# Kernel tuning notes

Measured on AMD Instinct MI355X. Metric: run time of the kernel, lower is better.

The kernel has to match this reference:

```python
import jax, jax.numpy as jnp
import numpy as np

N, E, G = 50000, 640000, 256
NODE_IN, EDGE_IN, H, L, T = 64, 16, 128, 4, 5
BN_EPS = 1e-5

def setup_inputs() -> dict:
    key = jax.random.key(0)
    ks = jax.random.split(key, 24)
    s = lambda k, shape, fan: jax.random.normal(k, shape, jnp.float32) * (1.0 / np.sqrt(fan))
    return {
        "x": jax.random.normal(ks[0], (N, NODE_IN), jnp.float32),
        "edge_attr": jax.random.normal(ks[1], (E, EDGE_IN), jnp.float32),
        "node_w": s(ks[2], (NODE_IN, H), NODE_IN), "node_b": jnp.zeros((H,), jnp.float32),
        "edge_w1": s(ks[3], (EDGE_IN, H), EDGE_IN), "edge_b1": jnp.zeros((H,), jnp.float32),
        "edge_w2": s(ks[4], (H, H), H), "edge_b2": jnp.zeros((H,), jnp.float32),
        "conv_w1": s(ks[5], (L, H, H), H), "conv_b1": jnp.zeros((L, H), jnp.float32),
        "conv_w2": s(ks[6], (L, H, H), H), "conv_b2": jnp.zeros((L, H), jnp.float32),
        "bn_gamma": jnp.ones((L, H), jnp.float32), "bn_beta": jnp.zeros((L, H), jnp.float32),
        "gate_w1": s(ks[7], (H, H // 2), H), "gate_b1": jnp.zeros((H // 2,), jnp.float32),
        "gate_w2": s(ks[8], (H // 2, 1), H // 2), "gate_b2": jnp.zeros((1,), jnp.float32),
        "head_w1": s(ks[9], (H, H), H), "head_b1": jnp.zeros((H,), jnp.float32),
        "head_w2": s(ks[10], (H, T), H), "head_b2": jnp.zeros((T,), jnp.float32),
        "edge_index": jax.random.randint(ks[11], (2, E), 0, N, jnp.int32),
        "batch": jnp.sort(jax.random.randint(ks[12], (N,), 0, G, jnp.int32)),
    }

def reference(x, edge_attr, node_w, node_b, edge_w1, edge_b1, edge_w2, edge_b2,
              conv_w1, conv_b1, conv_w2, conv_b2, bn_gamma, bn_beta,
              gate_w1, gate_b1, gate_w2, gate_b2, head_w1, head_b1, head_w2, head_b2,
              edge_index, batch):
    relu = jax.nn.relu
    h = x @ node_w + node_b                                   # [N,H]
    e = relu(edge_attr @ edge_w1 + edge_b1) @ edge_w2 + edge_b2  # [E,H]
    src, dst = edge_index[0], edge_index[1]
    bn_scale = 1.0 / jnp.sqrt(jnp.float32(1.0) + BN_EPS)      # eval BN: mean=0, var=1
    for l in range(L):
        m = relu(h[src] + e)                                  # GINEConv message [E,H]
        aggr = jax.ops.segment_sum(m, dst, num_segments=N)    # scatter-add
        z = h + aggr                                          # eps=0: (1+eps)*x + aggr
        z = relu(z @ conv_w1[l] + conv_b1[l]) @ conv_w2[l] + conv_b2[l]
        z = z * bn_scale * bn_gamma[l] + bn_beta[l]
        h = relu(z)                                           # dropout off (eval)
    gate = relu(h @ gate_w1 + gate_b1) @ gate_w2 + gate_b2    # [N,1]
    gmax = jax.ops.segment_max(gate, batch, num_segments=G)   # segment softmax
    wexp = jnp.exp(gate - gmax[batch])
    denom = jax.ops.segment_sum(wexp, batch, num_segments=G)
    alpha = wexp / denom[batch]
    g = jax.ops.segment_sum(alpha * h, batch, num_segments=G) # [G,H]
    return relu(g @ head_w1 + head_b1) @ head_w2 + head_b2    # [G,T]
```

## Files before the change

kernel.cpp:

```cpp
#include <hip/hip_runtime.h>

typedef unsigned short u16;
typedef __bf16 bf16x8 __attribute__((ext_vector_type(8)));
typedef float f32x4 __attribute__((ext_vector_type(4)));
typedef unsigned short u16x8 __attribute__((ext_vector_type(8)));

#define NNODES 50000
#define NEDGES 640000
#define NGRAPH 256

__device__ __forceinline__ float bf2f(u16 u) {
  unsigned int v = ((unsigned int)u) << 16; float f; __builtin_memcpy(&f, &v, 4); return f;
}
__device__ __forceinline__ u16 f2bf(float f) {
  unsigned int x; __builtin_memcpy(&x, &f, 4);
  unsigned int lsb = (x >> 16) & 1u;
  x += 0x7fffu + lsb;
  return (u16)(x >> 16);
}

__global__ void write_zero_f32(float* __restrict__ out, int n) {
  int i = blockIdx.x * 256 + threadIdx.x;
  if (i < n) out[i] = 0.f;
}

__global__ void prep_weights(const float* __restrict__ node_w, const float* __restrict__ edge_w1,
                             const float* __restrict__ edge_w2, const float* __restrict__ conv_w1,
                             const float* __restrict__ conv_w2, const float* __restrict__ gate_w1,
                             u16* __restrict__ node_wt, u16* __restrict__ edge_w1t,
                             u16* __restrict__ edge_w2t, u16* __restrict__ conv_w1t,
                             u16* __restrict__ conv_w2t, u16* __restrict__ gate_w1t,
                             int* __restrict__ counts, int* __restrict__ gcounts) {
  int o = blockIdx.x * 256 + threadIdx.x;
  if (o < NNODES) counts[o] = 0;
  if (o < NGRAPH) gcounts[o] = 0;
  if (o < 8192) { int n = o >> 6, k = o & 63; node_wt[o] = f2bf(node_w[k * 128 + n]); return; }
  o -= 8192;
  if (o < 4096) { int n = o >> 5, k = o & 31;
                  edge_w1t[o] = (k < 16) ? f2bf(edge_w1[k * 128 + n]) : (u16)0; return; }
  o -= 4096;
  if (o < 16384) { int n = o >> 7, k = o & 127; edge_w2t[o] = f2bf(edge_w2[k * 128 + n]); return; }
  o -= 16384;
  if (o < 65536) { int l = o >> 14, r = o & 16383, n = r >> 7, k = r & 127;
                   conv_w1t[o] = f2bf(conv_w1[l * 16384 + k * 128 + n]); return; }
  o -= 65536;
  if (o < 65536) { int l = o >> 14, r = o & 16383, n = r >> 7, k = r & 127;
                   conv_w2t[o] = f2bf(conv_w2[l * 16384 + k * 128 + n]); return; }
  o -= 65536;
  if (o < 8192) { int n = o >> 7, k = o & 127; gate_w1t[o] = f2bf(gate_w1[k * 64 + n]); }
}

__global__ void hist_all(const int* __restrict__ dst, const int* __restrict__ b,
                         int* __restrict__ counts, int* __restrict__ gc, int n) {
  int i = blockIdx.x * 256 + threadIdx.x;
  atomicAdd(&counts[dst[i]], 1);
  if (i < n) atomicAdd(&gc[b[i]], 1);
}
__global__ void scan_a(const int* __restrict__ counts, int* __restrict__ bsums,
                       const int* __restrict__ gcounts, int* __restrict__ goffs, int n) {
  __shared__ int sh4[4];
  int b = blockIdx.x, t = threadIdx.x;
  int lane = t & 63, w = t >> 6;
  if (b == 49) {
    int v = gcounts[t];
    int x = v;
    for (int d = 1; d < 64; d <<= 1) { int y = __shfl_up(x, (unsigned)d, 64); if (lane >= d) x += y; }
    if (lane == 63) sh4[w] = x;
    __syncthreads();
    int add = 0;
    for (int i = 0; i < w; i++) add += sh4[i];
    int incl = add + x;
    goffs[t] = incl - v;
    if (t == 255) goffs[256] = incl;
    return;
  }
  int i0 = b * 1024 + t * 4;
  int s = 0;
#pragma unroll
  for (int j = 0; j < 4; j++) { int i = i0 + j; if (i < n) s += counts[i]; }
  for (int m = 32; m; m >>= 1) s += __shfl_xor(s, m, 64);
  if (lane == 0) sh4[w] = s;
  __syncthreads();
  if (t == 0) bsums[b] = sh4[0] + sh4[1] + sh4[2] + sh4[3];
}
__global__ void scan_c(const int* __restrict__ counts, const int* __restrict__ bsums,
                       int* __restrict__ offs, int* __restrict__ cursor, int n) {
  int b = blockIdx.x, t = threadIdx.x;
  int i0 = b * 1024 + t * 4;
  int v[4]; int s = 0;
#pragma unroll
  for (int j = 0; j < 4; j++) { v[j] = (i0 + j < n) ? counts[i0 + j] : 0; s += v[j]; }
  int lane = t & 63, w = t >> 6;
  int x = s;
  for (int d = 1; d < 64; d <<= 1) { int y = __shfl_up(x, (unsigned)d, 64); if (lane >= d) x += y; }
  __shared__ int wt_[4];
  if (lane == 63) wt_[w] = x;
  __syncthreads();
  int add = 0;
  for (int i = 0; i < b; i++) add += bsums[i];
  for (int i = 0; i < w; i++) add += wt_[i];
  int excl = add + x - s;
#pragma unroll
  for (int j = 0; j < 4; j++) {
    int i = i0 + j;
    if (i < n) { offs[i] = excl; cursor[i] = excl; }
    excl += v[j];
  }
  if (b == 0 && t == 0) offs[n] = NEDGES;
}
__global__ void scatter_csr(const int* __restrict__ src, const int* __restrict__ dst,
                            int* __restrict__ cursor, int* __restrict__ csr_src,
                            int* __restrict__ csr_eid) {
  int i = blockIdx.x * 256 + threadIdx.x;
  int d = dst[i];
  int p = atomicAdd(&cursor[d], 1);
  csr_src[p] = src[i];
  csr_eid[p] = i;
}

template <int KB, int SA, int SB>
__device__ __forceinline__ void mfma_block(const u16* aL, const u16* bL, int m, int quad,
                                           int rbase, f32x4* acc) {
#pragma unroll
  for (int kb = 0; kb < KB; ++kb) {
    bf16x8 a = *(const bf16x8*)(aL + (rbase + m) * SA + kb * 32 + quad * 8);
#pragma unroll
    for (int nt = 0; nt < 8; ++nt) {
      bf16x8 b = *(const bf16x8*)(bL + (nt * 16 + m) * SB + kb * 32 + quad * 8);
      acc[nt] = __builtin_amdgcn_mfma_f32_16x16x32_bf16(a, b, acc[nt], 0, 0, 0);
    }
  }
}

__global__ __launch_bounds__(256) void node_encode(const float* __restrict__ x,
                                                   const u16* __restrict__ wt,
                                                   const float* __restrict__ nb,
                                                   u16* __restrict__ hb, int n) {
  __shared__ alignas(16) u16 sA[64 * 72];
  __shared__ alignas(16) u16 sW[128 * 72];
  int t = threadIdx.x;
  int row0 = blockIdx.x * 64;
#pragma unroll
  for (int i = 0; i < 4; i++) {
    int idx = t + 256 * i; int r = idx >> 4, c = idx & 15;
    int grow = row0 + r; if (grow > n - 1) grow = n - 1;
    float4 v = *(const float4*)(x + (size_t)grow * 64 + c * 4);
    ushort4 o; o.x = f2bf(v.x); o.y = f2bf(v.y); o.z = f2bf(v.z); o.w = f2bf(v.w);
    *(ushort4*)&sA[r * 72 + c * 4] = o;
  }
#pragma unroll
  for (int i = 0; i < 4; i++) {
    int idx = t + 256 * i; int nr = idx >> 3, c = idx & 7;
    *(uint4*)&sW[nr * 72 + c * 8] = *(const uint4*)(wt + nr * 64 + c * 8);
  }
  __syncthreads();
  int lane = t & 63, w = t >> 6, m = lane & 15, quad = lane >> 4, rbase = w * 16;
  f32x4 acc[8];
  f32x4 z4 = {0.f, 0.f, 0.f, 0.f};
#pragma unroll
  for (int i = 0; i < 8; i++) acc[i] = z4;
  mfma_block<2, 72, 72>(sA, sW, m, quad, rbase, acc);
#pragma unroll
  for (int nt = 0; nt < 8; nt++) {
    int col = nt * 16 + m;
    float bb = nb[col];
    f32x4 a4 = acc[nt];
#pragma unroll
    for (int r = 0; r < 4; r++) {
      int grow = row0 + rbase + quad * 4 + r;
      if (grow < n) hb[(size_t)grow * 128 + col] = f2bf(a4[r] + bb);
    }
  }
}

__global__ __launch_bounds__(256) void edge_encode(const float* __restrict__ ea,
                                                   const u16* __restrict__ w1t,
                                                   const u16* __restrict__ w2t,
                                                   const float* __restrict__ b1,
                                                   const float* __restrict__ b2,
                                                   const int* __restrict__ csr_eid,
                                                   u16* __restrict__ e_perm) {
  __shared__ alignas(16) u16 sA[128 * 48];
  __shared__ alignas(16) u16 sMid[128 * 136];
  int t = threadIdx.x;
  int lane = t & 63, w = t >> 6, m = lane & 15, quad = lane >> 4;
  int s0 = blockIdx.x * 128;
  int ebase = w * 32;

  {
    int r = lane >> 1, c = lane & 1;
    uint4 z = {0, 0, 0, 0};
    *(uint4*)&sA[(ebase + r) * 48 + 16 + c * 8] = z;
    int eidv = 0;
    if (lane < 32) eidv = csr_eid[s0 + ebase + lane];
    int eid = __shfl(eidv, r, 64);
    float4 v0 = *(const float4*)(ea + (size_t)eid * 16 + c * 8);
    float4 v1 = *(const float4*)(ea + (size_t)eid * 16 + c * 8 + 4);
    ushort4 o0; o0.x = f2bf(v0.x); o0.y = f2bf(v0.y); o0.z = f2bf(v0.z); o0.w = f2bf(v0.w);
    ushort4 o1; o1.x = f2bf(v1.x); o1.y = f2bf(v1.y); o1.z = f2bf(v1.z); o1.w = f2bf(v1.w);
    *(ushort4*)&sA[(ebase + r) * 48 + c * 8] = o0;
    *(ushort4*)&sA[(ebase + r) * 48 + c * 8 + 4] = o1;
  }
  bf16x8 w1f[8];
#pragma unroll
  for (int nt = 0; nt < 8; nt++)
    w1f[nt] = *(const bf16x8*)(w1t + (nt * 16 + m) * 32 + quad * 8);

  f32x4 z4 = {0.f, 0.f, 0.f, 0.f};
  f32x4 acc1[16];
#pragma unroll
  for (int i = 0; i < 16; i++) acc1[i] = z4;
#pragma unroll
  for (int rt2 = 0; rt2 < 2; rt2++) {
    bf16x8 a = *(const bf16x8*)(&sA[(ebase + rt2 * 16 + m) * 48 + quad * 8]);
#pragma unroll
    for (int nt = 0; nt < 8; nt++)
      acc1[rt2 * 8 + nt] = __builtin_amdgcn_mfma_f32_16x16x32_bf16(w1f[nt], a, acc1[rt2 * 8 + nt], 0, 0, 0);
  }
#pragma unroll
  for (int rt2 = 0; rt2 < 2; rt2++) {
#pragma unroll
    for (int nt = 0; nt < 8; nt++) {
      float4 bb = *(const float4*)&b1[nt * 16 + quad * 4];
      f32x4 a4 = acc1[rt2 * 8 + nt];
      u16 q0 = f2bf(fmaxf(a4[0] + bb.x, 0.f));
      u16 q1 = f2bf(fmaxf(a4[1] + bb.y, 0.f));
      u16 q2 = f2bf(fmaxf(a4[2] + bb.z, 0.f));
      u16 q3 = f2bf(fmaxf(a4[3] + bb.w, 0.f));
      uint2 pk;
      pk.x = (unsigned int)q0 | ((unsigned int)q1 << 16);
      pk.y = (unsigned int)q2 | ((unsigned int)q3 << 16);
      *(uint2*)&sMid[(ebase + rt2 * 16 + m) * 136 + nt * 16 + quad * 4] = pk;
    }
  }
  bf16x8 w2f[8];
  float4 b2v[2];
#pragma unroll
  for (int ct = 0; ct < 2; ct++) {
    b2v[ct] = *(const float4*)&b2[w * 32 + ct * 16 + quad * 4];
#pragma unroll
    for (int kb = 0; kb < 4; kb++)
      w2f[ct * 4 + kb] = *(const bf16x8*)(w2t + (size_t)(w * 32 + ct * 16 + m) * 128 + kb * 32 + quad * 8);
  }
  __syncthreads();

  f32x4 acc2[16];
#pragma unroll
  for (int i = 0; i < 16; i++) acc2[i] = z4;
#pragma unroll
  for (int rt = 0; rt < 8; rt++) {
#pragma unroll
    for (int kb = 0; kb < 4; kb++) {
      bf16x8 a = *(const bf16x8*)(&sMid[(rt * 16 + m) * 136 + kb * 32 + quad * 8]);
      acc2[rt * 2 + 0] = __builtin_amdgcn_mfma_f32_16x16x32_bf16(w2f[kb], a, acc2[rt * 2 + 0], 0, 0, 0);
      acc2[rt * 2 + 1] = __builtin_amdgcn_mfma_f32_16x16x32_bf16(w2f[4 + kb], a, acc2[rt * 2 + 1], 0, 0, 0);
    }
  }
  __syncthreads();
#pragma unroll
  for (int rt = 0; rt < 8; rt++) {
#pragma unroll
    for (int ct = 0; ct < 2; ct++) {
      f32x4 a4 = acc2[rt * 2 + ct];
      u16 q0 = f2bf(a4[0] + b2v[ct].x);
      u16 q1 = f2bf(a4[1] + b2v[ct].y);
      u16 q2 = f2bf(a4[2] + b2v[ct].z);
      u16 q3 = f2bf(a4[3] + b2v[ct].w);
      uint2 pk;
      pk.x = (unsigned int)q0 | ((unsigned int)q1 << 16);
      pk.y = (unsigned int)q2 | ((unsigned int)q3 << 16);
      *(uint2*)&sMid[(rt * 16 + m) * 136 + w * 32 + ct * 16 + quad * 4] = pk;
    }
  }
  __syncthreads();
#pragma unroll
  for (int i = 0; i < 8; i++) {
    int idx = t + 256 * i; int r = idx >> 4, c = idx & 15;
    *(uint4*)(e_perm + (size_t)(s0 + r) * 128 + c * 8) = *(const uint4*)&sMid[r * 136 + c * 8];
  }
}

__global__ __launch_bounds__(256) void layer_k(const u16* __restrict__ hin,
                                               u16* __restrict__ hout,
                                               const u16* __restrict__ e_perm,
                                               const int* __restrict__ offs,
                                               const int* __restrict__ csr_src,
                                               const u16* __restrict__ w1t, const u16* __restrict__ w2t,
                                               const float* __restrict__ b1, const float* __restrict__ b2,
                                               const float* __restrict__ gam, const float* __restrict__ bet,
                                               int n) {
  __shared__ alignas(16) u16 sZ[64 * 136];
  __shared__ alignas(16) u16 sMid[64 * 136];
  int t = threadIdx.x;
  int lane = t & 63, w = t >> 6, m = lane & 15, quad = lane >> 4;
  int row0 = blockIdx.x * 64;
  int li = m, q = quad;

  for (int k = 0; k < 16; k++) {
    int lr = w * 16 + k;
    int nd = row0 + lr; if (nd > n - 1) nd = n - 1;
    int e0 = offs[nd], e1 = offs[nd + 1];
    u16x8 hv = {};
    if (q == 0) hv = *(const u16x8*)(hin + (size_t)nd * 128 + li * 8);
    float a[8];
#pragma unroll
    for (int j = 0; j < 8; j++) a[j] = 0.f;
    int s = e0 + q;
    for (; s + 8 <= e1; s += 8) {
      int v0 = csr_src[s], v1 = csr_src[s + 4];
      u16x8 h0 = *(const u16x8*)(hin + (size_t)v0 * 128 + li * 8);
      u16x8 ee0 = *(const u16x8*)(e_perm + (size_t)s * 128 + li * 8);
      u16x8 h1 = *(const u16x8*)(hin + (size_t)v1 * 128 + li * 8);
      u16x8 ee1 = *(const u16x8*)(e_perm + (size_t)(s + 4) * 128 + li * 8);
#pragma unroll
      for (int j = 0; j < 8; j++) {
        a[j] += fmaxf(bf2f(h0[j]) + bf2f(ee0[j]), 0.f);
        a[j] += fmaxf(bf2f(h1[j]) + bf2f(ee1[j]), 0.f);
      }
    }
    for (; s < e1; s += 4) {
      int v = csr_src[s];
      u16x8 hgv = *(const u16x8*)(hin + (size_t)v * 128 + li * 8);
      u16x8 ev = *(const u16x8*)(e_perm + (size_t)s * 128 + li * 8);
#pragma unroll
      for (int j = 0; j < 8; j++) a[j] += fmaxf(bf2f(hgv[j]) + bf2f(ev[j]), 0.f);
    }
#pragma unroll
    for (int j = 0; j < 8; j++) {
      a[j] += __shfl_xor(a[j], 16, 64);
      a[j] += __shfl_xor(a[j], 32, 64);
    }
    if (q == 0) {
      u16x8 o;
#pragma unroll
      for (int j = 0; j < 8; j++) o[j] = f2bf(bf2f(hv[j]) + a[j]);
      *(u16x8*)&sZ[lr * 136 + li * 8] = o;
    }
  }
  bf16x8 w1f[8];
  float4 b1v[2];
#pragma unroll
  for (int ct = 0; ct < 2; ct++) {
    b1v[ct] = *(const float4*)&b1[w * 32 + ct * 16 + quad * 4];
#pragma unroll
    for (int kb = 0; kb < 4; kb++)
      w1f[ct * 4 + kb] = *(const bf16x8*)(w1t + (size_t)(w * 32 + ct * 16 + m) * 128 + kb * 32 + quad * 8);
  }
  __syncthreads();

  f32x4 z4 = {0.f, 0.f, 0.f, 0.f};
  f32x4 acc[8];
#pragma unroll
  for (int i = 0; i < 8; i++) acc[i] = z4;
#pragma unroll
  for (int rt = 0; rt < 4; rt++) {
#pragma unroll
    for (int kb = 0; kb < 4; kb++) {
      bf16x8 a = *(const bf16x8*)(&sZ[(rt * 16 + m) * 136 + kb * 32 + quad * 8]);
      acc[rt * 2 + 0] = __builtin_amdgcn_mfma_f32_16x16x32_bf16(w1f[kb], a, acc[rt * 2 + 0], 0, 0, 0);
      acc[rt * 2 + 1] = __builtin_amdgcn_mfma_f32_16x16x32_bf16(w1f[4 + kb], a, acc[rt * 2 + 1], 0, 0, 0);
    }
  }
#pragma unroll
  for (int rt = 0; rt < 4; rt++) {
#pragma unroll
    for (int ct = 0; ct < 2; ct++) {
      f32x4 a4 = acc[rt * 2 + ct];
      u16 q0 = f2bf(fmaxf(a4[0] + b1v[ct].x, 0.f));
      u16 q1 = f2bf(fmaxf(a4[1] + b1v[ct].y, 0.f));
      u16 q2 = f2bf(fmaxf(a4[2] + b1v[ct].z, 0.f));
      u16 q3 = f2bf(fmaxf(a4[3] + b1v[ct].w, 0.f));
      uint2 pk;
      pk.x = (unsigned int)q0 | ((unsigned int)q1 << 16);
      pk.y = (unsigned int)q2 | ((unsigned int)q3 << 16);
      *(uint2*)&sMid[(rt * 16 + m) * 136 + w * 32 + ct * 16 + quad * 4] = pk;
    }
  }
  bf16x8 w2f[8];
  float4 b2v[2], gamv[2], betv[2];
#pragma unroll
  for (int ct = 0; ct < 2; ct++) {
    int c0 = w * 32 + ct * 16 + quad * 4;
    b2v[ct] = *(const float4*)&b2[c0];
    gamv[ct] = *(const float4*)&gam[c0];
    betv[ct] = *(const float4*)&bet[c0];
#pragma unroll
    for (int kb = 0; kb < 4; kb++)
      w2f[ct * 4 + kb] = *(const bf16x8*)(w2t + (size_t)c0 / 4 * 0 + (size_t)(w * 32 + ct * 16 + m) * 128 + kb * 32 + quad * 8);
  }
  __syncthreads();

  f32x4 acc2[8];
#pragma unroll
  for (int i = 0; i < 8; i++) acc2[i] = z4;
#pragma unroll
  for (int rt = 0; rt < 4; rt++) {
#pragma unroll
    for (int kb = 0; kb < 4; kb++) {
      bf16x8 a = *(const bf16x8*)(&sMid[(rt * 16 + m) * 136 + kb * 32 + quad * 8]);
      acc2[rt * 2 + 0] = __builtin_amdgcn_mfma_f32_16x16x32_bf16(w2f[kb], a, acc2[rt * 2 + 0], 0, 0, 0);
      acc2[rt * 2 + 1] = __builtin_amdgcn_mfma_f32_16x16x32_bf16(w2f[4 + kb], a, acc2[rt * 2 + 1], 0, 0, 0);
    }
  }
  const float bns = 0.99999500003749983f;
#pragma unroll
  for (int rt = 0; rt < 4; rt++) {
#pragma unroll
    for (int ct = 0; ct < 2; ct++) {
      f32x4 a4 = acc2[rt * 2 + ct];
      u16 q0 = f2bf(fmaxf((a4[0] + b2v[ct].x) * bns * gamv[ct].x + betv[ct].x, 0.f));
      u16 q1 = f2bf(fmaxf((a4[1] + b2v[ct].y) * bns * gamv[ct].y + betv[ct].y, 0.f));
      u16 q2 = f2bf(fmaxf((a4[2] + b2v[ct].z) * bns * gamv[ct].z + betv[ct].z, 0.f));
      u16 q3 = f2bf(fmaxf((a4[3] + b2v[ct].w) * bns * gamv[ct].w + betv[ct].w, 0.f));
      uint2 pk;
      pk.x = (unsigned int)q0 | ((unsigned int)q1 << 16);
      pk.y = (unsigned int)q2 | ((unsigned int)q3 << 16);
      *(uint2*)&sZ[(rt * 16 + m) * 136 + w * 32 + ct * 16 + quad * 4] = pk;
    }
  }
  __syncthreads();
#pragma unroll
  for (int i = 0; i < 4; i++) {
    int idx = t + 256 * i; int r = idx >> 4, c = idx & 15;
    int grow = row0 + r;
    if (grow < n)
      *(uint4*)(hout + (size_t)grow * 128 + c * 8) = *(const uint4*)&sZ[r * 136 + c * 8];
  }
}

__global__ __launch_bounds__(256) void gate_k(const u16* __restrict__ hb,
                                              const u16* __restrict__ w1t,
                                              const float* __restrict__ b1,
                                              const float* __restrict__ w2,
                                              const float* __restrict__ b2,
                                              float* __restrict__ gate, int n) {
  __shared__ alignas(16) u16 sA[64 * 136];
  __shared__ alignas(16) u16 sW[64 * 136];
  int t = threadIdx.x;
  int row0 = blockIdx.x * 64;
#pragma unroll
  for (int i = 0; i < 4; i++) {
    int idx = t + 256 * i; int r = idx >> 4, c = idx & 15;
    int grow = row0 + r; if (grow > n - 1) grow = n - 1;
    *(uint4*)&sA[r * 136 + c * 8] = *(const uint4*)(hb + (size_t)grow * 128 + c * 8);
  }
#pragma unroll
  for (int i = 0; i < 4; i++) {
    int idx = t + 256 * i; int r = idx >> 4, c = idx & 15;
    *(uint4*)&sW[r * 136 + c * 8] = *(const uint4*)(w1t + r * 128 + c * 8);
  }
  __syncthreads();
  int lane = t & 63, w = t >> 6, m = lane & 15, quad = lane >> 4, rbase = w * 16;
  f32x4 z4 = {0.f, 0.f, 0.f, 0.f};
  f32x4 acc[4];
#pragma unroll
  for (int i = 0; i < 4; i++) acc[i] = z4;
#pragma unroll
  for (int kb = 0; kb < 4; kb++) {
    bf16x8 a = *(const bf16x8*)(&sA[(rbase + m) * 136 + kb * 32 + quad * 8]);
#pragma unroll
    for (int nt = 0; nt < 4; nt++) {
      bf16x8 b = *(const bf16x8*)(&sW[(nt * 16 + m) * 136 + kb * 32 + quad * 8]);
      acc[nt] = __builtin_amdgcn_mfma_f32_16x16x32_bf16(a, b, acc[nt], 0, 0, 0);
    }
  }
  float b1v[4], w2v[4];
#pragma unroll
  for (int nt = 0; nt < 4; nt++) { b1v[nt] = b1[nt * 16 + m]; w2v[nt] = w2[nt * 16 + m]; }
  float b2v = b2[0];
#pragma unroll
  for (int r = 0; r < 4; r++) {
    float p = 0.f;
#pragma unroll
    for (int nt = 0; nt < 4; nt++) p += fmaxf(acc[nt][r] + b1v[nt], 0.f) * w2v[nt];
    p += __shfl_xor(p, 1, 64);
    p += __shfl_xor(p, 2, 64);
    p += __shfl_xor(p, 4, 64);
    p += __shfl_xor(p, 8, 64);
    if (m == 0) {
      int grow = row0 + rbase + quad * 4 + r;
      if (grow < n) gate[grow] = p + b2v;
    }
  }
}

__global__ __launch_bounds__(256) void pool_k(const float* __restrict__ gate,
                                              const u16* __restrict__ hb,
                                              const int* __restrict__ goffs,
                                              float* __restrict__ gpool) {
  int g = blockIdx.x, t = threadIdx.x;
  int s0 = goffs[g], s1 = goffs[g + 1];
  int lane = t & 63, w = t >> 6;
  __shared__ float red[4];
  __shared__ float fin[2][128];
  float mx = -3.4e38f;
  for (int i = s0 + t; i < s1; i += 256) mx = fmaxf(mx, gate[i]);
  for (int d = 32; d; d >>= 1) mx = fmaxf(mx, __shfl_xor(mx, d, 64));
  if (lane == 0) red[w] = mx;
  __syncthreads();
  mx = fmaxf(fmaxf(red[0], red[1]), fmaxf(red[2], red[3]));
  __syncthreads();
  float sm = 0.f;
  for (int i = s0 + t; i < s1; i += 256) sm += __expf(gate[i] - mx);
  for (int d = 32; d; d >>= 1) sm += __shfl_xor(sm, d, 64);
  if (lane == 0) red[w] = sm;
  __syncthreads();
  sm = red[0] + red[1] + red[2] + red[3];
  int g2 = t >> 7, tc = t & 127;
  float acc = 0.f;
  for (int i = s0 + g2; i < s1; i += 2)
    acc += __expf(gate[i] - mx) * bf2f(hb[(size_t)i * 128 + tc]);
  fin[g2][tc] = acc;
  __syncthreads();
  if (t < 128) gpool[g * 128 + t] = (s1 > s0) ? (fin[0][t] + fin[1][t]) / sm : 0.f;
}

__global__ __launch_bounds__(128) void head_k(const float* __restrict__ gpool,
                                              const float* __restrict__ w1, const float* __restrict__ b1,
                                              const float* __restrict__ w2, const float* __restrict__ b2,
                                              float* __restrict__ out) {
  int g = blockIdx.x, t = threadIdx.x;
  __shared__ float sg[128];
  __shared__ float shid[128];
  sg[t] = gpool[g * 128 + t];
  __syncthreads();
  float s = 0.f;
  for (int k = 0; k < 128; k++) s += sg[k] * w1[k * 128 + t];
  shid[t] = fmaxf(s + b1[t], 0.f);
  __syncthreads();
  if (t < 5) {
    float o = b2[t];
    for (int k = 0; k < 128; k++) o += shid[k] * w2[k * 5 + t];
    out[g * 5 + t] = o;
  }
}

extern "C" void kernel_launch(void* const* d_in, const int* in_sizes, int n_in,
                              void* d_out, int out_size, void* d_ws, size_t ws_size,
                              hipStream_t stream) {
  const int N = NNODES, E = NEDGES, G = NGRAPH;
  const float* x = (const float*)d_in[0];
  const float* edge_attr = (const float*)d_in[1];
  const float* node_w = (const float*)d_in[2];
  const float* node_b = (const float*)d_in[3];
  const float* edge_w1 = (const float*)d_in[4];
  const float* edge_b1 = (const float*)d_in[5];
  const float* edge_w2 = (const float*)d_in[6];
  const float* edge_b2 = (const float*)d_in[7];
  const float* conv_w1 = (const float*)d_in[8];
  const float* conv_b1 = (const float*)d_in[9];
  const float* conv_w2 = (const float*)d_in[10];
  const float* conv_b2 = (const float*)d_in[11];
  const float* bn_gamma = (const float*)d_in[12];
  const float* bn_beta = (const float*)d_in[13];
  const float* gate_w1 = (const float*)d_in[14];
  const float* gate_b1 = (const float*)d_in[15];
  const float* gate_w2 = (const float*)d_in[16];
  const float* gate_b2 = (const float*)d_in[17];
  const float* head_w1 = (const float*)d_in[18];
  const float* head_b1 = (const float*)d_in[19];
  const float* head_w2 = (const float*)d_in[20];
  const float* head_b2 = (const float*)d_in[21];
  const int* eidx = (const int*)d_in[22];
  const int* batch = (const int*)d_in[23];
  const int* esrc = eidx;
  const int* edst = eidx + E;

  char* wp = (char*)d_ws;
  auto alloc = [&](size_t bytes) { char* p = wp; wp += (bytes + 255) & ~(size_t)255; return p; };
  u16* e_perm = (u16*)alloc((size_t)E * 128 * 2);
  u16* hb = (u16*)alloc((size_t)(N + 16) * 128 * 2);
  u16* hb2 = (u16*)alloc((size_t)(N + 16) * 128 * 2);
  float* gate = (float*)alloc((size_t)N * 4);
  float* gpool = (float*)alloc((size_t)G * 128 * 4);
  int* counts = (int*)alloc((size_t)N * 4);
  int* offs = (int*)alloc((size_t)(N + 1) * 4);
  int* cursor = (int*)alloc((size_t)N * 4);
  int* csr_src = (int*)alloc((size_t)E * 4);
  int* csr_eid = (int*)alloc((size_t)E * 4);
  int* bsums = (int*)alloc(64 * 4);
  int* gcounts = (int*)alloc(G * 4);
  int* goffs = (int*)alloc((G + 1) * 4);
  u16* node_wt = (u16*)alloc(8192 * 2);
  u16* edge_w1t = (u16*)alloc(4096 * 2);
  u16* edge_w2t = (u16*)alloc(16384 * 2);
  u16* conv_w1t = (u16*)alloc(65536 * 2);
  u16* conv_w2t = (u16*)alloc(65536 * 2);
  u16* gate_w1t = (u16*)alloc(8192 * 2);

  size_t need = (size_t)(wp - (char*)d_ws);
  if (need > ws_size) {
    write_zero_f32<<<(out_size + 255) / 256, 256, 0, stream>>>((float*)d_out, out_size);
    return;
  }

  prep_weights<<<656, 256, 0, stream>>>(node_w, edge_w1, edge_w2, conv_w1, conv_w2, gate_w1,
                                        node_wt, edge_w1t, edge_w2t, conv_w1t, conv_w2t, gate_w1t,
                                        counts, gcounts);
  hist_all<<<E / 256, 256, 0, stream>>>(edst, batch, counts, gcounts, N);
  scan_a<<<50, 256, 0, stream>>>(counts, bsums, gcounts, goffs, N);
  scan_c<<<49, 256, 0, stream>>>(counts, bsums, offs, cursor, N);
  scatter_csr<<<E / 256, 256, 0, stream>>>(esrc, edst, cursor, csr_src, csr_eid);
  node_encode<<<(N + 63) / 64, 256, 0, stream>>>(x, node_wt, node_b, hb, N);
  edge_encode<<<E / 128, 256, 0, stream>>>(edge_attr, edge_w1t, edge_w2t, edge_b1, edge_b2,
                                           csr_eid, e_perm);
  u16* hcur = hb;
  u16* hnext = hb2;
  for (int l = 0; l < 4; l++) {
    layer_k<<<(N + 63) / 64, 256, 0, stream>>>(hcur, hnext, e_perm, offs, csr_src,
                                               conv_w1t + l * 16384, conv_w2t + l * 16384,
                                               conv_b1 + l * 128, conv_b2 + l * 128,
                                               bn_gamma + l * 128, bn_beta + l * 128, N);
    u16* tmp = hcur; hcur = hnext; hnext = tmp;
  }
  gate_k<<<(N + 63) / 64, 256, 0, stream>>>(hcur, gate_w1t, gate_b1, gate_w2, gate_b2, gate, N);
  pool_k<<<G, 256, 0, stream>>>(gate, hcur, goffs, gpool);
  head_k<<<G, 128, 0, stream>>>(gpool, head_w1, head_b1, head_w2, head_b2, (float*)d_out);
}
```

Baseline: 646.2 us.

## Build CSR with chunked shared-memory histograms instead of global atomics

Replaces the global-atomic histogram and cursor-based scatter with a two-level scheme. Blocks own a 4096-node chunk and one of 16 edge slices, count destinations in LDS, and write per-slice partial counts that scan_a turns into per-slice offsets. The scatter then places edges using LDS atomics, which also makes the CSR order deterministic. Graph offsets now come from a binary search on the sorted batch array, and layer_k loads its row offsets once per wave and broadcasts them with shuffles. In exchange, each of the 13 chunks rescans the whole dst array in both hist and scatter, and the partial array adds 16×N ints of traffic.

```diff
diff --git a/kernel.cpp b/kernel.cpp
--- a/kernel.cpp
+++ b/kernel.cpp
@@ -8,6 +8,9 @@
 #define NNODES 50000
 #define NEDGES 640000
 #define NGRAPH 256
+#define HCHUNK 4096
+#define HSPLIT 16
+#define NCHUNK 13
 
 __device__ __forceinline__ float bf2f(u16 u) {
   unsigned int v = ((unsigned int)u) << 16; float f; __builtin_memcpy(&f, &v, 4); return f;
@@ -29,11 +32,8 @@
                              const float* __restrict__ conv_w2, const float* __restrict__ gate_w1,
                              u16* __restrict__ node_wt, u16* __restrict__ edge_w1t,
                              u16* __restrict__ edge_w2t, u16* __restrict__ conv_w1t,
-                             u16* __restrict__ conv_w2t, u16* __restrict__ gate_w1t,
-                             int* __restrict__ counts, int* __restrict__ gcounts) {
+                             u16* __restrict__ conv_w2t, u16* __restrict__ gate_w1t) {
   int o = blockIdx.x * 256 + threadIdx.x;
-  if (o < NNODES) counts[o] = 0;
-  if (o < NGRAPH) gcounts[o] = 0;
   if (o < 8192) { int n = o >> 6, k = o & 63; node_wt[o] = f2bf(node_w[k * 128 + n]); return; }
   o -= 8192;
   if (o < 4096) { int n = o >> 5, k = o & 31;
@@ -50,41 +50,65 @@
   if (o < 8192) { int n = o >> 7, k = o & 127; gate_w1t[o] = f2bf(gate_w1[k * 64 + n]); }
 }
 
-__global__ void hist_all(const int* __restrict__ dst, const int* __restrict__ b,
-                         int* __restrict__ counts, int* __restrict__ gc, int n) {
-  int i = blockIdx.x * 256 + threadIdx.x;
-  atomicAdd(&counts[dst[i]], 1);
-  if (i < n) atomicAdd(&gc[b[i]], 1);
-}
-__global__ void scan_a(const int* __restrict__ counts, int* __restrict__ bsums,
-                       const int* __restrict__ gcounts, int* __restrict__ goffs, int n) {
+__global__ __launch_bounds__(256) void hist_k(const int* __restrict__ dst,
+                                              int* __restrict__ partial) {
+  __shared__ int hloc[HCHUNK];
+  int b = blockIdx.x, t = threadIdx.x;
+  int c = b >> 4, sp = b & 15;
+  for (int j = t; j < HCHUNK; j += 256) hloc[j] = 0;
+  __syncthreads();
+  int base = c * HCHUNK;
+  int e0 = sp * (NEDGES / HSPLIT), e1 = e0 + NEDGES / HSPLIT;
+  for (int i = e0 + t; i < e1; i += 256) {
+    int d = dst[i] - base;
+    if ((unsigned)d < HCHUNK) atomicAdd(&hloc[d], 1);
+  }
+  __syncthreads();
+  for (int j = t; j < HCHUNK; j += 256) {
+    int g = base + j;
+    if (g < NNODES) partial[sp * NNODES + g] = hloc[j];
+  }
+}
+__global__ __launch_bounds__(256) void scan_a(int* __restrict__ partial,
+                                              int* __restrict__ counts,
+                                              int* __restrict__ bsums,
+                                              const int* __restrict__ batch,
+                                              int* __restrict__ goffs, int n) {
   __shared__ int sh4[4];
   int b = blockIdx.x, t = threadIdx.x;
   int lane = t & 63, w = t >> 6;
   if (b == 49) {
-    int v = gcounts[t];
-    int x = v;
-    for (int d = 1; d < 64; d <<= 1) { int y = __shfl_up(x, (unsigned)d, 64); if (lane >= d) x += y; }
-    if (lane == 63) sh4[w] = x;
-    __syncthreads();
-    int add = 0;
-    for (int i = 0; i < w; i++) add += sh4[i];
-    int incl = add + x;
-    goffs[t] = incl - v;
-    if (t == 255) goffs[256] = incl;
+    int lo = 0, hi = n;
+    while (lo < hi) { int mid = (lo + hi) >> 1; if (batch[mid] < t) lo = mid + 1; else hi = mid; }
+    goffs[t] = lo;
+    if (t == 0) goffs[256] = n;
     return;
   }
   int i0 = b * 1024 + t * 4;
   int s = 0;
 #pragma unroll
-  for (int j = 0; j < 4; j++) { int i = i0 + j; if (i < n) s += counts[i]; }
+  for (int j = 0; j < 4; j++) {
+    int g = i0 + j;
+    if (g < n) {
+      int run = 0;
+#pragma unroll
+      for (int sp = 0; sp < HSPLIT; sp++) {
+        int v = partial[sp * NNODES + g];
+        partial[sp * NNODES + g] = run;
+        run += v;
+      }
+      counts[g] = run;
+      s += run;
+    }
+  }
   for (int m = 32; m; m >>= 1) s += __shfl_xor(s, m, 64);
   if (lane == 0) sh4[w] = s;
   __syncthreads();
   if (t == 0) bsums[b] = sh4[0] + sh4[1] + sh4[2] + sh4[3];
 }
-__global__ void scan_c(const int* __restrict__ counts, const int* __restrict__ bsums,
-                       int* __restrict__ offs, int* __restrict__ cursor, int n) {
+__global__ __launch_bounds__(256) void scan_c(const int* __restrict__ counts,
+                                              const int* __restrict__ bsums,
+                                              int* __restrict__ offs, int n) {
   int b = blockIdx.x, t = threadIdx.x;
   int i0 = b * 1024 + t * 4;
   int v[4]; int s = 0;
@@ -103,19 +127,34 @@
 #pragma unroll
   for (int j = 0; j < 4; j++) {
     int i = i0 + j;
-    if (i < n) { offs[i] = excl; cursor[i] = excl; }
+    if (i < n) offs[i] = excl;
     excl += v[j];
   }
   if (b == 0 && t == 0) offs[n] = NEDGES;
 }
-__global__ void scatter_csr(const int* __restrict__ src, const int* __restrict__ dst,
-                            int* __restrict__ cursor, int* __restrict__ csr_src,
-                            int* __restrict__ csr_eid) {
-  int i = blockIdx.x * 256 + threadIdx.x;
-  int d = dst[i];
-  int p = atomicAdd(&cursor[d], 1);
-  csr_src[p] = src[i];
-  csr_eid[p] = i;
+__global__ __launch_bounds__(256) void scatter_k(const int* __restrict__ src,
+                                                 const int* __restrict__ dst,
+                                                 const int* __restrict__ offs,
+                                                 const int* __restrict__ partial,
+                                                 int* __restrict__ csr_src,
+                                                 int* __restrict__ csr_eid) {
+  __shared__ int hloc[HCHUNK];
+  int b = blockIdx.x, t = threadIdx.x;
+  int c = b >> 4, sp = b & 15;
+  for (int j = t; j < HCHUNK; j += 256) hloc[j] = 0;
+  __syncthreads();
+  int base = c * HCHUNK;
+  int e0 = sp * (NEDGES / HSPLIT), e1 = e0 + NEDGES / HSPLIT;
+  for (int i = e0 + t; i < e1; i += 256) {
+    int d = dst[i];
+    int dl = d - base;
+    if ((unsigned)dl < HCHUNK) {
+      int r = atomicAdd(&hloc[dl], 1);
+      int p = offs[d] + partial[sp * NNODES + d] + r;
+      csr_src[p] = src[i];
+      csr_eid[p] = i;
+    }
+  }
 }
 
 template <int KB, int SA, int SB>
@@ -296,12 +335,16 @@
   int row0 = blockIdx.x * 64;
   int li = m, q = quad;
 
+  int oidx = row0 + w * 16 + (lane < 16 ? lane : 16);
+  if (oidx > n) oidx = n;
+  int offv = offs[oidx];
+
   for (int k = 0; k < 16; k++) {
-    int lr = w * 16 + k;
-    int nd = row0 + lr; if (nd > n - 1) nd = n - 1;
-    int e0 = offs[nd], e1 = offs[nd + 1];
+    int nd = row0 + w * 16 + k;
+    int ndc = (nd > n - 1) ? (n - 1) : nd;
+    int e0 = __shfl(offv, k, 64), e1 = __shfl(offv, k + 1, 64);
     u16x8 hv = {};
-    if (q == 0) hv = *(const u16x8*)(hin + (size_t)nd * 128 + li * 8);
+    if (q == 0) hv = *(const u16x8*)(hin + (size_t)ndc * 128 + li * 8);
     float a[8];
 #pragma unroll
     for (int j = 0; j < 8; j++) a[j] = 0.f;
@@ -334,7 +377,7 @@
       u16x8 o;
 #pragma unroll
       for (int j = 0; j < 8; j++) o[j] = f2bf(bf2f(hv[j]) + a[j]);
-      *(u16x8*)&sZ[lr * 136 + li * 8] = o;
+      *(u16x8*)&sZ[(w * 16 + k) * 136 + li * 8] = o;
     }
   }
   bf16x8 w1f[8];
@@ -386,7 +429,7 @@
     betv[ct] = *(const float4*)&bet[c0];
 #pragma unroll
     for (int kb = 0; kb < 4; kb++)
-      w2f[ct * 4 + kb] = *(const bf16x8*)(w2t + (size_t)c0 / 4 * 0 + (size_t)(w * 32 + ct * 16 + m) * 128 + kb * 32 + quad * 8);
+      w2f[ct * 4 + kb] = *(const bf16x8*)(w2t + (size_t)(w * 32 + ct * 16 + m) * 128 + kb * 32 + quad * 8);
   }
   __syncthreads();
 
@@ -575,11 +618,10 @@
   float* gpool = (float*)alloc((size_t)G * 128 * 4);
   int* counts = (int*)alloc((size_t)N * 4);
   int* offs = (int*)alloc((size_t)(N + 1) * 4);
-  int* cursor = (int*)alloc((size_t)N * 4);
+  int* partial = (int*)alloc((size_t)HSPLIT * N * 4);
   int* csr_src = (int*)alloc((size_t)E * 4);
   int* csr_eid = (int*)alloc((size_t)E * 4);
   int* bsums = (int*)alloc(64 * 4);
-  int* gcounts = (int*)alloc(G * 4);
   int* goffs = (int*)alloc((G + 1) * 4);
   u16* node_wt = (u16*)alloc(8192 * 2);
   u16* edge_w1t = (u16*)alloc(4096 * 2);
@@ -595,12 +637,11 @@
   }
 
   prep_weights<<<656, 256, 0, stream>>>(node_w, edge_w1, edge_w2, conv_w1, conv_w2, gate_w1,
-                                        node_wt, edge_w1t, edge_w2t, conv_w1t, conv_w2t, gate_w1t,
-                                        counts, gcounts);
-  hist_all<<<E / 256, 256, 0, stream>>>(edst, batch, counts, gcounts, N);
-  scan_a<<<50, 256, 0, stream>>>(counts, bsums, gcounts, goffs, N);
-  scan_c<<<49, 256, 0, stream>>>(counts, bsums, offs, cursor, N);
-  scatter_csr<<<E / 256, 256, 0, stream>>>(esrc, edst, cursor, csr_src, csr_eid);
+                                        node_wt, edge_w1t, edge_w2t, conv_w1t, conv_w2t, gate_w1t);
+  hist_k<<<NCHUNK * HSPLIT, 256, 0, stream>>>(edst, partial);
+  scan_a<<<50, 256, 0, stream>>>(partial, counts, bsums, batch, goffs, N);
+  scan_c<<<49, 256, 0, stream>>>(counts, bsums, offs, N);
+  scatter_k<<<NCHUNK * HSPLIT, 256, 0, stream>>>(esrc, edst, offs, partial, csr_src, csr_eid);
   node_encode<<<(N + 63) / 64, 256, 0, stream>>>(x, node_wt, node_b, hb, N);
   edge_encode<<<E / 128, 256, 0, stream>>>(edge_attr, edge_w1t, edge_w2t, edge_b1, edge_b2,
                                            csr_eid, e_perm);
```

Result: slower. 679.7 us (+5.2%).
